# Performance work log

Measured on AMD Instinct MI355X. Metric: run time of the kernel, lower is better.

Reference implementation:

```python
import jax, jax.numpy as jnp
import numpy as np


def setup_inputs() -> dict:
    key = jax.random.key(0)
    ks = jax.random.split(key, 8)
    B, T, H, Hu = 128, 64, 1024, 512
    MJW = 64                    # max_jump_width
    J = 2 * MJW + 1             # size_jump_width_set_nn = 129
    N = 2 * T                   # HMM states (word states + null states)
    I = 64                      # source sentence length
    sc = 0.02
    return {
        "y_hidden": jax.random.normal(ks[0], (B, T, H), jnp.float32),
        # emission probs p(source word i | state s), strictly positive for log
        "emission": jax.random.uniform(ks[1], (B, N, I), jnp.float32, 1e-4, 1.0),
        "source_lengths": jax.random.randint(ks[2], (B,), 1, I + 1),
        "W1": jax.random.normal(ks[3], (H, Hu), jnp.float32) * sc,
        "b1": jnp.zeros((Hu,), jnp.float32),
        "W2": jax.random.normal(ks[4], (Hu, J), jnp.float32) * sc,
        "b2": jnp.zeros((J,), jnp.float32),
        "W3": jax.random.normal(ks[5], (Hu, 1), jnp.float32) * sc,
        "b3": jnp.zeros((1,), jnp.float32),
        "max_jump_width": MJW,
    }


def _build_transition(y_hidden, W1, b1, W2, b2, W3, b3, mjw):
    # Dense(tanh) -> Dense softmax jump-width distribution + Dense sigmoid p0
    B, T, _ = y_hidden.shape
    ts = jnp.tanh(y_hidden @ W1 + b1)                       # [B,T,Hu]
    jw = jax.nn.softmax(ts @ W2 + b2, axis=-1)              # [B,T,J]
    p0 = jax.nn.sigmoid(jnp.squeeze(ts @ W3 + b3, -1))      # [B,T]
    r = jnp.arange(T)
    # banded gather: transition[i, j] = jw[i, mjw + j - i]
    band_idx = mjw + r[None, :] - r[:, None]                # [T,T], in [0, J)
    band = jnp.take_along_axis(jw, band_idx[None], axis=2)  # [B,T,T]
    diag_p0 = jnp.eye(T, dtype=jw.dtype) * p0[:, :, None]   # [B,T,T]
    top = jnp.concatenate([band, diag_p0], axis=2)          # [B,T,2T]
    return jnp.concatenate([top, top], axis=1)              # [B,2T,2T]


def _forward_alignment(transition, emission, source_lengths):
    # Faithful translation of the tf.scan forward algorithm. tf.scan with no
    # initializer uses elems[0] as the initial accumulator and emits it as
    # output[0] (log part = ones, so the [0,0] element is 1.0).
    B, N, I = emission.shape
    em = jnp.transpose(emission, (2, 0, 1))                 # [I,B,N]
    alpha0 = jnp.broadcast_to(em[0][:, None, :], (B, N, N)) # rows all equal e_0
    L0 = jnp.ones((B,), emission.dtype)

    def step(carry, e):
        alpha, L = carry                                    # [B,N,N], [B]
        yi = e[:, None, :]                                  # rows of yi_prob identical
        m1 = jnp.matmul(alpha, transition)                  # [B,N,N]
        tmp = m1 * yi
        tmp = tmp / jnp.sum(tmp, axis=2, keepdims=True)     # row-normalized alpha
        m2 = jnp.matmul(transition, alpha) * yi             # [B,N,N]
        max_j = jnp.max(m2, axis=-1)[:, 0]                  # gather row 0 -> [B]
        state_prev = jnp.sum(m1, axis=1)                    # [B,N]
        state = jnp.log(e) + jnp.log(state_prev) - max_j[:, None]
        state_log = jnp.log(jnp.sum(jnp.exp(state), axis=-1))
        L_new = L + state_log + max_j                       # [B]
        return (tmp, L_new), L_new

    (_, _), logs = jax.lax.scan(step, (alpha0, L0), em[1:])  # [I-1,B]
    logs = jnp.concatenate([L0[None], logs], axis=0).T       # [B,I]
    idx = (source_lengths - 1)[:, None]
    return jnp.take_along_axis(logs, idx, axis=1)[:, 0]      # [B]


def reference(y_hidden, emission, source_lengths, W1, b1, W2, b2, W3, b3, max_jump_width):
    transition = _build_transition(y_hidden, W1, b1, W2, b2, W3, b3, max_jump_width)
    return _forward_alignment(transition, emission, source_lengths)
```

## Files before the change

kernel.cpp:

```cpp
#include <hip/hip_runtime.h>
#include <hip/hip_bf16.h>

typedef float f32x4 __attribute__((ext_vector_type(4)));
typedef __bf16 bf16x8 __attribute__((ext_vector_type(8)));
typedef unsigned short u16;

#define OFF_W1T  0u
#define OFF_W23B 1048576u
#define OFF_TS   1196032u

static __device__ __forceinline__ u16 f2bf(float x) {
    __bf16 h = (__bf16)x;
    return __builtin_bit_cast(u16, h);
}

__device__ __forceinline__ void gload16(const void* g, void* l) {
    __builtin_amdgcn_global_load_lds(
        (const __attribute__((address_space(1))) void*)g,
        (__attribute__((address_space(3))) void*)l,
        16, 0, 0);
}

__global__ __launch_bounds__(256) void prep_kernel(
    const float* __restrict__ W1, const float* __restrict__ W2,
    const float* __restrict__ W3,
    __bf16* __restrict__ W1T, __bf16* __restrict__ W23B)
{
    const int t = threadIdx.x;
    if (blockIdx.x < 128) {
        __shared__ __bf16 lds_t[64][72];
        const int kt = blockIdx.x >> 3, nt = blockIdx.x & 7;
        const int k0 = kt * 64, n0 = nt * 64;
        {
            const int kr = t >> 2, c0 = (t & 3) * 16;
            const float* src = W1 + (size_t)(k0 + kr) * 512 + n0 + c0;
            #pragma unroll
            for (int q = 0; q < 4; ++q) {
                float4 v = *(const float4*)(src + q * 4);
                lds_t[kr][c0 + q * 4 + 0] = (__bf16)v.x;
                lds_t[kr][c0 + q * 4 + 1] = (__bf16)v.y;
                lds_t[kr][c0 + q * 4 + 2] = (__bf16)v.z;
                lds_t[kr][c0 + q * 4 + 3] = (__bf16)v.w;
            }
        }
        __syncthreads();
        {
            const int nr = t >> 2, kc = (t & 3) * 16;
            bf16x8 o0, o1;
            #pragma unroll
            for (int j = 0; j < 8; ++j) o0[j] = lds_t[kc + j][nr];
            #pragma unroll
            for (int j = 0; j < 8; ++j) o1[j] = lds_t[kc + 8 + j][nr];
            __bf16* dst = W1T + (size_t)(n0 + nr) * 1024 + k0 + kc;
            *(bf16x8*)(dst)     = o0;
            *(bf16x8*)(dst + 8) = o1;
        }
    } else {
        int g = (blockIdx.x - 128) * 256 + t;
        if (g < 9216) {
            int n = g >> 6;
            int k8 = (g & 63) * 8;
            bf16x8 v;
            #pragma unroll
            for (int j = 0; j < 8; ++j) {
                int k = k8 + j;
                float x = 0.0f;
                if (n < 129) x = W2[(size_t)k * 129 + n];
                else if (n == 129) x = W3[k];
                v[j] = (__bf16)x;
            }
            int kk = k8 >> 5, lg = (k8 >> 3) & 3, ct = n >> 4, lr = n & 15;
            *(bf16x8*)&W23B[(((size_t)(kk * 9 + ct)) * 64 + lg * 16 + lr) * 8] = v;
        }
    }
}

__global__ __launch_bounds__(256, 2) void gemm1_kernel(
    const float* __restrict__ Y, const __bf16* __restrict__ W1T,
    const float* __restrict__ b1, u16* __restrict__ ts)
{
    __shared__ float  As[3][64 * 32];
    __shared__ __bf16 Bs[3][128 * 32];
    const int tid = threadIdx.x;
    const int m0 = blockIdx.x * 64, n0 = blockIdx.y * 128;
    const int wid = tid >> 6, lane = tid & 63;
    const int wr = wid >> 1, wc = wid & 1;
    const int lr = lane & 15, lg = lane >> 4;

    const int al = lane >> 3;
    const int au = (lane & 7) ^ al;
    const float* yA0 = Y + (size_t)(m0 + (wid * 2 + 0) * 8 + al) * 1024 + au * 4;
    const float* yA1 = Y + (size_t)(m0 + (wid * 2 + 1) * 8 + al) * 1024 + au * 4;
    const int bl = lane >> 2;
    const int bu = (lane & 3) ^ (bl & 3);
    const __bf16* wB0 = W1T + (size_t)(n0 + (wid * 2 + 0) * 16 + bl) * 1024 + bu * 8;
    const __bf16* wB1 = W1T + (size_t)(n0 + (wid * 2 + 1) * 16 + bl) * 1024 + bu * 8;

    f32x4 acc[2][4];
    #pragma unroll
    for (int m = 0; m < 2; m++)
        #pragma unroll
        for (int n = 0; n < 4; n++) { f32x4 z = {0.f,0.f,0.f,0.f}; acc[m][n] = z; }

#define STAGE(buf, kt) do { \
    gload16(yA0 + (kt) * 32, &As[buf][(wid * 2 + 0) * 256]); \
    gload16(yA1 + (kt) * 32, &As[buf][(wid * 2 + 1) * 256]); \
    gload16(wB0 + (kt) * 32, &Bs[buf][(wid * 2 + 0) * 512]); \
    gload16(wB1 + (kt) * 32, &Bs[buf][(wid * 2 + 1) * 512]); \
} while (0)

#define COMPUTE(buf) do { \
    bf16x8 af[2]; bf16x8 bfr[4]; \
    _Pragma("unroll") \
    for (int m = 0; m < 2; ++m) { \
        const int row = wr * 32 + m * 16 + lr; \
        const int r7 = row & 7; \
        float4 h0 = *(const float4*)&As[buf][row * 32 + (((lg * 2 + 0) ^ r7) * 4)]; \
        float4 h1 = *(const float4*)&As[buf][row * 32 + (((lg * 2 + 1) ^ r7) * 4)]; \
        bf16x8 tt; \
        tt[0]=(__bf16)h0.x; tt[1]=(__bf16)h0.y; tt[2]=(__bf16)h0.z; tt[3]=(__bf16)h0.w; \
        tt[4]=(__bf16)h1.x; tt[5]=(__bf16)h1.y; tt[6]=(__bf16)h1.z; tt[7]=(__bf16)h1.w; \
        af[m] = tt; \
    } \
    _Pragma("unroll") \
    for (int n = 0; n < 4; ++n) { \
        const int rowb = wc * 64 + n * 16 + lr; \
        bfr[n] = *(const bf16x8*)&Bs[buf][rowb * 32 + ((lg ^ (rowb & 3)) * 8)]; \
    } \
    __builtin_amdgcn_s_setprio(1); \
    _Pragma("unroll") \
    for (int m = 0; m < 2; ++m) \
        _Pragma("unroll") \
        for (int n = 0; n < 4; ++n) \
            acc[m][n] = __builtin_amdgcn_mfma_f32_16x16x32_bf16(af[m], bfr[n], acc[m][n], 0, 0, 0); \
    __builtin_amdgcn_s_setprio(0); \
} while (0)

#define KSTEP(buf, kt, VM, DO_STAGE) do { \
    asm volatile("s_waitcnt vmcnt(" #VM ")" ::: "memory"); \
    __builtin_amdgcn_s_barrier(); \
    COMPUTE(buf); \
    asm volatile("s_waitcnt lgkmcnt(0)" ::: "memory"); \
    __builtin_amdgcn_s_barrier(); \
    if (DO_STAGE) STAGE(buf, (kt) + 3); \
} while (0)

    STAGE(0, 0); STAGE(1, 1); STAGE(2, 2);
    #pragma unroll 1
    for (int base = 0; base < 27; base += 3) {
        KSTEP(0, base + 0, 8, 1);
        KSTEP(1, base + 1, 8, 1);
        KSTEP(2, base + 2, 8, 1);
    }
    KSTEP(0, 27, 8, 1);
    KSTEP(1, 28, 8, 1);
    KSTEP(2, 29, 8, 0);
    KSTEP(0, 30, 4, 0);
    KSTEP(1, 31, 0, 0);

    #pragma unroll
    for (int m = 0; m < 2; m++) {
        #pragma unroll
        for (int n = 0; n < 4; n++) {
            int col = n0 + wc * 64 + n * 16 + lr;
            float bias = b1[col];
            #pragma unroll
            for (int j = 0; j < 4; j++) {
                int row = m0 + wr * 32 + m * 16 + lg * 4 + j;
                float v = tanhf(acc[m][n][j] + bias);
                ts[(size_t)row * 512 + col] = f2bf(v);
            }
        }
    }
#undef STAGE
#undef COMPUTE
#undef KSTEP
}

__global__ __launch_bounds__(256, 1) void gemm2_recur_kernel(
    const u16* __restrict__ ts, const u16* __restrict__ W23B,
    const float* __restrict__ b2, const float* __restrict__ b3,
    const float* __restrict__ em, const int* __restrict__ slen,
    float* __restrict__ out)
{
    __shared__ float jwT_s[64][65];
    __shared__ float em_s[128][65];
    __shared__ float p0_s[64];
    __shared__ f32x4 a_bc4[16];
    const int b = blockIdx.x;
    const int tid = threadIdx.x;
    const int w = tid >> 6, lane = tid & 63;
    const int lr = lane & 15, lg = lane >> 4;
    const int r0 = b * 64 + w * 16;

    {
        const float4* eg = (const float4*)(em + (size_t)b * 8192);
        #pragma unroll
        for (int q = 0; q < 8; ++q) {
            int i4 = tid + q * 256;
            float4 v = eg[i4];
            int base = i4 * 4; int n = base >> 6; int ii = base & 63;
            em_s[n][ii] = v.x; em_s[n][ii + 1] = v.y; em_s[n][ii + 2] = v.z; em_s[n][ii + 3] = v.w;
        }
    }

    f32x4 acc[9];
    #pragma unroll
    for (int ct = 0; ct < 9; ct++) { f32x4 z = {0.f,0.f,0.f,0.f}; acc[ct] = z; }

    #pragma unroll 4
    for (int kk = 0; kk < 16; ++kk) {
        bf16x8 a = *(const bf16x8*)(ts + (size_t)(r0 + lr) * 512 + kk * 32 + lg * 8);
        #pragma unroll
        for (int ct = 0; ct < 9; ct++) {
            bf16x8 bv = *(const bf16x8*)(W23B + ((size_t)(kk * 9 + ct) * 64 + lane) * 8);
            acc[ct] = __builtin_amdgcn_mfma_f32_16x16x32_bf16(a, bv, acc[ct], 0, 0, 0);
        }
    }

    float b3v = b3[0];
    #pragma unroll
    for (int j = 0; j < 4; j++) {
        int rloc = w * 16 + lg * 4 + j;
        float v[9];
        float mx = -1e30f;
        #pragma unroll
        for (int ct = 0; ct < 9; ct++) {
            int col = ct * 16 + lr;
            if (col < 129) { float x = acc[ct][j] + b2[col]; v[ct] = x; mx = fmaxf(mx, x); }
            else v[ct] = -1e30f;
        }
        #pragma unroll
        for (int o = 1; o < 16; o <<= 1) mx = fmaxf(mx, __shfl_xor(mx, o));
        float sum = 0.f;
        #pragma unroll
        for (int ct = 0; ct < 9; ct++) {
            int col = ct * 16 + lr;
            if (col < 129) { float e = expf(v[ct] - mx); v[ct] = e; sum += e; }
        }
        #pragma unroll
        for (int o = 1; o < 16; o <<= 1) sum += __shfl_xor(sum, o);
        float inv = 1.0f / sum;
        #pragma unroll
        for (int ct = 0; ct < 9; ct++) {
            int col = ct * 16 + lr;
            int cc = col - 64 + rloc;
            if (col < 129 && cc >= 0 && cc < 64)
                jwT_s[cc][rloc] = v[ct] * inv;
        }
        if (lr == 1) {
            float pv = acc[8][j] + b3v;
            p0_s[rloc] = 1.0f / (1.0f + expf(-pv));
        }
    }
    __syncthreads();
    if (tid >= 64) return;

    const int c = tid;
    f32x4 B0  = *(const f32x4*)&jwT_s[c][0];
    f32x4 B1  = *(const f32x4*)&jwT_s[c][4];
    f32x4 B2  = *(const f32x4*)&jwT_s[c][8];
    f32x4 B3  = *(const f32x4*)&jwT_s[c][12];
    f32x4 B4  = *(const f32x4*)&jwT_s[c][16];
    f32x4 B5  = *(const f32x4*)&jwT_s[c][20];
    f32x4 B6  = *(const f32x4*)&jwT_s[c][24];
    f32x4 B7  = *(const f32x4*)&jwT_s[c][28];
    f32x4 B8  = *(const f32x4*)&jwT_s[c][32];
    f32x4 B9  = *(const f32x4*)&jwT_s[c][36];
    f32x4 B10 = *(const f32x4*)&jwT_s[c][40];
    f32x4 B11 = *(const f32x4*)&jwT_s[c][44];
    f32x4 B12 = *(const f32x4*)&jwT_s[c][48];
    f32x4 B13 = *(const f32x4*)&jwT_s[c][52];
    f32x4 B14 = *(const f32x4*)&jwT_s[c][56];
    f32x4 B15 = *(const f32x4*)&jwT_s[c][60];
    const float p0r = p0_s[c];
    const int idx = slen[b] - 1;

    unsigned rbase = (unsigned)(uintptr_t)(__attribute__((address_space(3))) void*)&a_bc4[0];
    unsigned waddr = rbase + (unsigned)c * 4u;

    float ut = em_s[c][0] + em_s[c + 64][0];
    float Lacc = 0.f;

    #pragma unroll 1
    for (int i = 1; i <= idx; ++i) {
        float aloc = ut;
        f32x4 A0,A1,A2,A3,A4,A5,A6,A7,A8,A9,A10,A11,A12,A13,A14,A15;
        asm volatile(
            "ds_write_b32 %17, %16\n\t"
            "s_waitcnt lgkmcnt(0)\n\t"
            "ds_read_b128 %0, %18 offset:0\n\t"
            "ds_read_b128 %1, %18 offset:16\n\t"
            "ds_read_b128 %2, %18 offset:32\n\t"
            "ds_read_b128 %3, %18 offset:48\n\t"
            "ds_read_b128 %4, %18 offset:64\n\t"
            "ds_read_b128 %5, %18 offset:80\n\t"
            "ds_read_b128 %6, %18 offset:96\n\t"
            "ds_read_b128 %7, %18 offset:112\n\t"
            "ds_read_b128 %8, %18 offset:128\n\t"
            "ds_read_b128 %9, %18 offset:144\n\t"
            "ds_read_b128 %10, %18 offset:160\n\t"
            "ds_read_b128 %11, %18 offset:176\n\t"
            "ds_read_b128 %12, %18 offset:192\n\t"
            "ds_read_b128 %13, %18 offset:208\n\t"
            "ds_read_b128 %14, %18 offset:224\n\t"
            "ds_read_b128 %15, %18 offset:240\n\t"
            "s_waitcnt lgkmcnt(0)"
            : "=&v"(A0), "=&v"(A1), "=&v"(A2),  "=&v"(A3),
              "=&v"(A4), "=&v"(A5), "=&v"(A6),  "=&v"(A7),
              "=&v"(A8), "=&v"(A9), "=&v"(A10), "=&v"(A11),
              "=&v"(A12),"=&v"(A13),"=&v"(A14), "=&v"(A15)
            : "v"(ut), "v"(waddr), "v"(rbase)
            : "memory");
        float s0 = 0.f, s1 = 0.f, s2 = 0.f, s3 = 0.f;
#define ACC4(AV, BV) do { \
        s0 = fmaf((AV)[0], (BV)[0], s0); \
        s1 = fmaf((AV)[1], (BV)[1], s1); \
        s2 = fmaf((AV)[2], (BV)[2], s2); \
        s3 = fmaf((AV)[3], (BV)[3], s3); \
} while (0)
        ACC4(A0, B0);   ACC4(A1, B1);   ACC4(A2, B2);   ACC4(A3, B3);
        ACC4(A4, B4);   ACC4(A5, B5);   ACC4(A6, B6);   ACC4(A7, B7);
        ACC4(A8, B8);   ACC4(A9, B9);   ACC4(A10, B10); ACC4(A11, B11);
        ACC4(A12, B12); ACC4(A13, B13); ACC4(A14, B14); ACC4(A15, B15);
#undef ACC4
        ut = ((s0 + s1) + (s2 + s3)) * em_s[c][i] + aloc * p0r * em_s[c + 64][i];
        if (((i & 3) == 0) || (i == idx)) {
            float r = ut;
            #pragma unroll
            for (int o = 1; o < 64; o <<= 1) r += __shfl_xor(r, o);
            Lacc += __log2f(r);
            ut *= __builtin_amdgcn_rcpf(r);
        }
    }
    if (c == 0) out[b] = 1.0f + 0.6931471805599453f * (Lacc + 7.0f * (float)idx);
}

extern "C" void kernel_launch(void* const* d_in, const int* in_sizes, int n_in,
                              void* d_out, int out_size, void* d_ws, size_t ws_size,
                              hipStream_t stream)
{
    const float* Y   = (const float*)d_in[0];
    const float* em  = (const float*)d_in[1];
    const int*   sl  = (const int*)d_in[2];
    const float* W1  = (const float*)d_in[3];
    const float* b1  = (const float*)d_in[4];
    const float* W2  = (const float*)d_in[5];
    const float* b2  = (const float*)d_in[6];
    const float* W3  = (const float*)d_in[7];
    const float* b3  = (const float*)d_in[8];
    float* out = (float*)d_out;
    char* ws = (char*)d_ws;

    __bf16* W1T  = (__bf16*)(ws + OFF_W1T);
    __bf16* W23B = (__bf16*)(ws + OFF_W23B);
    u16*    ts   = (u16*)(ws + OFF_TS);

    prep_kernel<<<164, 256, 0, stream>>>(W1, W2, W3, W1T, W23B);
    dim3 g1(128, 4);
    gemm1_kernel<<<g1, 256, 0, stream>>>(Y, W1T, b1, ts);
    gemm2_recur_kernel<<<128, 256, 0, stream>>>(ts, (const u16*)W23B, b2, b3, em, sl, out);
}
```

Baseline: 83.07 us.

## Restructure pipeline: direct-load GEMM1, split band and recurrence kernels, exponent renormalization

Pre-packs W1 into an MFMA fragment layout so gemm1 loads operands straight from global memory into registers, dropping the LDS triple-buffer pipeline and its barriers. The fused gemm2+recurrence kernel is split into a band kernel that writes jw/p0 to workspace and a 64-thread recurrence kernel. Per-step renormalization now uses an exponent-bit rescale from lane 0 instead of a periodic wave reduction, log and reciprocal. This adds a kernel launch and a global round-trip, and gemm1 loses LDS staging and latency hiding.

```diff
diff --git a/kernel.cpp b/kernel.cpp
--- a/kernel.cpp
+++ b/kernel.cpp
@@ -5,58 +5,34 @@
 typedef __bf16 bf16x8 __attribute__((ext_vector_type(8)));
 typedef unsigned short u16;
 
-#define OFF_W1T  0u
+#define OFF_W1B  0u
 #define OFF_W23B 1048576u
 #define OFF_TS   1196032u
+#define OFF_JWT  9584640u
+#define OFF_P0   11681792u
 
 static __device__ __forceinline__ u16 f2bf(float x) {
     __bf16 h = (__bf16)x;
     return __builtin_bit_cast(u16, h);
 }
 
-__device__ __forceinline__ void gload16(const void* g, void* l) {
-    __builtin_amdgcn_global_load_lds(
-        (const __attribute__((address_space(1))) void*)g,
-        (__attribute__((address_space(3))) void*)l,
-        16, 0, 0);
-}
-
 __global__ __launch_bounds__(256) void prep_kernel(
     const float* __restrict__ W1, const float* __restrict__ W2,
     const float* __restrict__ W3,
-    __bf16* __restrict__ W1T, __bf16* __restrict__ W23B)
+    __bf16* __restrict__ W1B, __bf16* __restrict__ W23B)
 {
     const int t = threadIdx.x;
-    if (blockIdx.x < 128) {
-        __shared__ __bf16 lds_t[64][72];
-        const int kt = blockIdx.x >> 3, nt = blockIdx.x & 7;
-        const int k0 = kt * 64, n0 = nt * 64;
-        {
-            const int kr = t >> 2, c0 = (t & 3) * 16;
-            const float* src = W1 + (size_t)(k0 + kr) * 512 + n0 + c0;
-            #pragma unroll
-            for (int q = 0; q < 4; ++q) {
-                float4 v = *(const float4*)(src + q * 4);
-                lds_t[kr][c0 + q * 4 + 0] = (__bf16)v.x;
-                lds_t[kr][c0 + q * 4 + 1] = (__bf16)v.y;
-                lds_t[kr][c0 + q * 4 + 2] = (__bf16)v.z;
-                lds_t[kr][c0 + q * 4 + 3] = (__bf16)v.w;
-            }
-        }
-        __syncthreads();
-        {
-            const int nr = t >> 2, kc = (t & 3) * 16;
-            bf16x8 o0, o1;
-            #pragma unroll
-            for (int j = 0; j < 8; ++j) o0[j] = lds_t[kc + j][nr];
-            #pragma unroll
-            for (int j = 0; j < 8; ++j) o1[j] = lds_t[kc + 8 + j][nr];
-            __bf16* dst = W1T + (size_t)(n0 + nr) * 1024 + k0 + kc;
-            *(bf16x8*)(dst)     = o0;
-            *(bf16x8*)(dst + 8) = o1;
-        }
+    if (blockIdx.x < 256) {
+        int g = blockIdx.x * 256 + t;
+        int n = g & 511, k8 = g >> 9;
+        bf16x8 v;
+        #pragma unroll
+        for (int j = 0; j < 8; ++j)
+            v[j] = (__bf16)W1[(size_t)(k8 * 8 + j) * 512 + n];
+        int kt = k8 >> 2, lg = k8 & 3, ct = n >> 4, lr = n & 15;
+        *(bf16x8*)&W1B[(((size_t)(kt * 32 + ct)) * 64 + lg * 16 + lr) * 8] = v;
     } else {
-        int g = (blockIdx.x - 128) * 256 + t;
+        int g = (blockIdx.x - 256) * 256 + t;
         if (g < 9216) {
             int n = g >> 6;
             int k8 = (g & 63) * 8;
@@ -75,26 +51,20 @@
     }
 }
 
-__global__ __launch_bounds__(256, 2) void gemm1_kernel(
-    const float* __restrict__ Y, const __bf16* __restrict__ W1T,
+__global__ __launch_bounds__(256) void gemm1_kernel(
+    const float* __restrict__ Y, const u16* __restrict__ W1B,
     const float* __restrict__ b1, u16* __restrict__ ts)
 {
-    __shared__ float  As[3][64 * 32];
-    __shared__ __bf16 Bs[3][128 * 32];
     const int tid = threadIdx.x;
-    const int m0 = blockIdx.x * 64, n0 = blockIdx.y * 128;
+    const int m0 = blockIdx.x * 64, nb = blockIdx.y;
     const int wid = tid >> 6, lane = tid & 63;
     const int wr = wid >> 1, wc = wid & 1;
     const int lr = lane & 15, lg = lane >> 4;
 
-    const int al = lane >> 3;
-    const int au = (lane & 7) ^ al;
-    const float* yA0 = Y + (size_t)(m0 + (wid * 2 + 0) * 8 + al) * 1024 + au * 4;
-    const float* yA1 = Y + (size_t)(m0 + (wid * 2 + 1) * 8 + al) * 1024 + au * 4;
-    const int bl = lane >> 2;
-    const int bu = (lane & 3) ^ (bl & 3);
-    const __bf16* wB0 = W1T + (size_t)(n0 + (wid * 2 + 0) * 16 + bl) * 1024 + bu * 8;
-    const __bf16* wB1 = W1T + (size_t)(n0 + (wid * 2 + 1) * 16 + bl) * 1024 + bu * 8;
+    const float* ya0 = Y + (size_t)(m0 + wr * 32 + lr) * 1024 + lg * 8;
+    const float* ya1 = ya0 + (size_t)16 * 1024;
+    const int ct0 = nb * 8 + wc * 4;
+    const u16* wb = W1B + ((size_t)ct0 * 64 + lane) * 8;
 
     f32x4 acc[2][4];
     #pragma unroll
@@ -102,67 +72,37 @@
         #pragma unroll
         for (int n = 0; n < 4; n++) { f32x4 z = {0.f,0.f,0.f,0.f}; acc[m][n] = z; }
 
-#define STAGE(buf, kt) do { \
-    gload16(yA0 + (kt) * 32, &As[buf][(wid * 2 + 0) * 256]); \
-    gload16(yA1 + (kt) * 32, &As[buf][(wid * 2 + 1) * 256]); \
-    gload16(wB0 + (kt) * 32, &Bs[buf][(wid * 2 + 0) * 512]); \
-    gload16(wB1 + (kt) * 32, &Bs[buf][(wid * 2 + 1) * 512]); \
-} while (0)
-
-#define COMPUTE(buf) do { \
-    bf16x8 af[2]; bf16x8 bfr[4]; \
-    _Pragma("unroll") \
-    for (int m = 0; m < 2; ++m) { \
-        const int row = wr * 32 + m * 16 + lr; \
-        const int r7 = row & 7; \
-        float4 h0 = *(const float4*)&As[buf][row * 32 + (((lg * 2 + 0) ^ r7) * 4)]; \
-        float4 h1 = *(const float4*)&As[buf][row * 32 + (((lg * 2 + 1) ^ r7) * 4)]; \
-        bf16x8 tt; \
-        tt[0]=(__bf16)h0.x; tt[1]=(__bf16)h0.y; tt[2]=(__bf16)h0.z; tt[3]=(__bf16)h0.w; \
-        tt[4]=(__bf16)h1.x; tt[5]=(__bf16)h1.y; tt[6]=(__bf16)h1.z; tt[7]=(__bf16)h1.w; \
-        af[m] = tt; \
-    } \
-    _Pragma("unroll") \
-    for (int n = 0; n < 4; ++n) { \
-        const int rowb = wc * 64 + n * 16 + lr; \
-        bfr[n] = *(const bf16x8*)&Bs[buf][rowb * 32 + ((lg ^ (rowb & 3)) * 8)]; \
-    } \
-    __builtin_amdgcn_s_setprio(1); \
-    _Pragma("unroll") \
-    for (int m = 0; m < 2; ++m) \
-        _Pragma("unroll") \
-        for (int n = 0; n < 4; ++n) \
-            acc[m][n] = __builtin_amdgcn_mfma_f32_16x16x32_bf16(af[m], bfr[n], acc[m][n], 0, 0, 0); \
-    __builtin_amdgcn_s_setprio(0); \
-} while (0)
-
-#define KSTEP(buf, kt, VM, DO_STAGE) do { \
-    asm volatile("s_waitcnt vmcnt(" #VM ")" ::: "memory"); \
-    __builtin_amdgcn_s_barrier(); \
-    COMPUTE(buf); \
-    asm volatile("s_waitcnt lgkmcnt(0)" ::: "memory"); \
-    __builtin_amdgcn_s_barrier(); \
-    if (DO_STAGE) STAGE(buf, (kt) + 3); \
-} while (0)
-
-    STAGE(0, 0); STAGE(1, 1); STAGE(2, 2);
-    #pragma unroll 1
-    for (int base = 0; base < 27; base += 3) {
-        KSTEP(0, base + 0, 8, 1);
-        KSTEP(1, base + 1, 8, 1);
-        KSTEP(2, base + 2, 8, 1);
-    }
-    KSTEP(0, 27, 8, 1);
-    KSTEP(1, 28, 8, 1);
-    KSTEP(2, 29, 8, 0);
-    KSTEP(0, 30, 4, 0);
-    KSTEP(1, 31, 0, 0);
+    #pragma unroll 4
+    for (int kt = 0; kt < 32; ++kt) {
+        float4 p0v = *(const float4*)(ya0 + kt * 32);
+        float4 p1v = *(const float4*)(ya0 + kt * 32 + 4);
+        float4 q0v = *(const float4*)(ya1 + kt * 32);
+        float4 q1v = *(const float4*)(ya1 + kt * 32 + 4);
+        bf16x8 a0, a1;
+        a0[0]=(__bf16)p0v.x; a0[1]=(__bf16)p0v.y; a0[2]=(__bf16)p0v.z; a0[3]=(__bf16)p0v.w;
+        a0[4]=(__bf16)p1v.x; a0[5]=(__bf16)p1v.y; a0[6]=(__bf16)p1v.z; a0[7]=(__bf16)p1v.w;
+        a1[0]=(__bf16)q0v.x; a1[1]=(__bf16)q0v.y; a1[2]=(__bf16)q0v.z; a1[3]=(__bf16)q0v.w;
+        a1[4]=(__bf16)q1v.x; a1[5]=(__bf16)q1v.y; a1[6]=(__bf16)q1v.z; a1[7]=(__bf16)q1v.w;
+        const u16* wk = wb + (size_t)kt * 16384;
+        bf16x8 bf0 = *(const bf16x8*)(wk);
+        bf16x8 bf1 = *(const bf16x8*)(wk + 512);
+        bf16x8 bf2 = *(const bf16x8*)(wk + 1024);
+        bf16x8 bf3 = *(const bf16x8*)(wk + 1536);
+        acc[0][0] = __builtin_amdgcn_mfma_f32_16x16x32_bf16(a0, bf0, acc[0][0], 0, 0, 0);
+        acc[0][1] = __builtin_amdgcn_mfma_f32_16x16x32_bf16(a0, bf1, acc[0][1], 0, 0, 0);
+        acc[0][2] = __builtin_amdgcn_mfma_f32_16x16x32_bf16(a0, bf2, acc[0][2], 0, 0, 0);
+        acc[0][3] = __builtin_amdgcn_mfma_f32_16x16x32_bf16(a0, bf3, acc[0][3], 0, 0, 0);
+        acc[1][0] = __builtin_amdgcn_mfma_f32_16x16x32_bf16(a1, bf0, acc[1][0], 0, 0, 0);
+        acc[1][1] = __builtin_amdgcn_mfma_f32_16x16x32_bf16(a1, bf1, acc[1][1], 0, 0, 0);
+        acc[1][2] = __builtin_amdgcn_mfma_f32_16x16x32_bf16(a1, bf2, acc[1][2], 0, 0, 0);
+        acc[1][3] = __builtin_amdgcn_mfma_f32_16x16x32_bf16(a1, bf3, acc[1][3], 0, 0, 0);
+    }
 
     #pragma unroll
     for (int m = 0; m < 2; m++) {
         #pragma unroll
         for (int n = 0; n < 4; n++) {
-            int col = n0 + wc * 64 + n * 16 + lr;
+            int col = nb * 128 + wc * 64 + n * 16 + lr;
             float bias = b1[col];
             #pragma unroll
             for (int j = 0; j < 4; j++) {
@@ -172,38 +112,19 @@
             }
         }
     }
-#undef STAGE
-#undef COMPUTE
-#undef KSTEP
-}
-
-__global__ __launch_bounds__(256, 1) void gemm2_recur_kernel(
+}
+
+__global__ __launch_bounds__(256) void band_kernel(
     const u16* __restrict__ ts, const u16* __restrict__ W23B,
     const float* __restrict__ b2, const float* __restrict__ b3,
-    const float* __restrict__ em, const int* __restrict__ slen,
-    float* __restrict__ out)
-{
-    __shared__ float jwT_s[64][65];
-    __shared__ float em_s[128][65];
-    __shared__ float p0_s[64];
-    __shared__ f32x4 a_bc4[16];
+    float* __restrict__ jwT, float* __restrict__ p0)
+{
     const int b = blockIdx.x;
     const int tid = threadIdx.x;
     const int w = tid >> 6, lane = tid & 63;
     const int lr = lane & 15, lg = lane >> 4;
     const int r0 = b * 64 + w * 16;
 
-    {
-        const float4* eg = (const float4*)(em + (size_t)b * 8192);
-        #pragma unroll
-        for (int q = 0; q < 8; ++q) {
-            int i4 = tid + q * 256;
-            float4 v = eg[i4];
-            int base = i4 * 4; int n = base >> 6; int ii = base & 63;
-            em_s[n][ii] = v.x; em_s[n][ii + 1] = v.y; em_s[n][ii + 2] = v.z; em_s[n][ii + 3] = v.w;
-        }
-    }
-
     f32x4 acc[9];
     #pragma unroll
     for (int ct = 0; ct < 9; ct++) { f32x4 z = {0.f,0.f,0.f,0.f}; acc[ct] = z; }
@@ -246,41 +167,61 @@
             int col = ct * 16 + lr;
             int cc = col - 64 + rloc;
             if (col < 129 && cc >= 0 && cc < 64)
-                jwT_s[cc][rloc] = v[ct] * inv;
+                jwT[((size_t)b * 64 + cc) * 64 + rloc] = v[ct] * inv;
         }
         if (lr == 1) {
             float pv = acc[8][j] + b3v;
-            p0_s[rloc] = 1.0f / (1.0f + expf(-pv));
-        }
-    }
+            p0[b * 64 + rloc] = 1.0f / (1.0f + expf(-pv));
+        }
+    }
+}
+
+__global__ __launch_bounds__(64, 1) void recur_kernel(
+    const float* __restrict__ jwT, const float* __restrict__ p0g,
+    const float* __restrict__ em, const int* __restrict__ slen,
+    float* __restrict__ out)
+{
+    __shared__ float em_s[128][65];
+    __shared__ f32x4 a_bc4[16];
+    const int b = blockIdx.x, c = threadIdx.x;
+
+    const float* bb = jwT + ((size_t)b * 64 + c) * 64;
+    f32x4 B0  = *(const f32x4*)(bb + 0);
+    f32x4 B1  = *(const f32x4*)(bb + 4);
+    f32x4 B2  = *(const f32x4*)(bb + 8);
+    f32x4 B3  = *(const f32x4*)(bb + 12);
+    f32x4 B4  = *(const f32x4*)(bb + 16);
+    f32x4 B5  = *(const f32x4*)(bb + 20);
+    f32x4 B6  = *(const f32x4*)(bb + 24);
+    f32x4 B7  = *(const f32x4*)(bb + 28);
+    f32x4 B8  = *(const f32x4*)(bb + 32);
+    f32x4 B9  = *(const f32x4*)(bb + 36);
+    f32x4 B10 = *(const f32x4*)(bb + 40);
+    f32x4 B11 = *(const f32x4*)(bb + 44);
+    f32x4 B12 = *(const f32x4*)(bb + 48);
+    f32x4 B13 = *(const f32x4*)(bb + 52);
+    f32x4 B14 = *(const f32x4*)(bb + 56);
+    f32x4 B15 = *(const f32x4*)(bb + 60);
+
+    {
+        const float4* eg = (const float4*)(em + (size_t)b * 8192);
+        #pragma unroll 8
+        for (int q = 0; q < 32; ++q) {
+            int i4 = c + q * 64;
+            float4 v = eg[i4];
+            int base = i4 * 4; int n = base >> 6; int ii = base & 63;
+            em_s[n][ii] = v.x; em_s[n][ii + 1] = v.y; em_s[n][ii + 2] = v.z; em_s[n][ii + 3] = v.w;
+        }
+    }
+    const float p0r = p0g[b * 64 + c];
+    const int idx = slen[b] - 1;
     __syncthreads();
-    if (tid >= 64) return;
-
-    const int c = tid;
-    f32x4 B0  = *(const f32x4*)&jwT_s[c][0];
-    f32x4 B1  = *(const f32x4*)&jwT_s[c][4];
-    f32x4 B2  = *(const f32x4*)&jwT_s[c][8];
-    f32x4 B3  = *(const f32x4*)&jwT_s[c][12];
-    f32x4 B4  = *(const f32x4*)&jwT_s[c][16];
-    f32x4 B5  = *(const f32x4*)&jwT_s[c][20];
-    f32x4 B6  = *(const f32x4*)&jwT_s[c][24];
-    f32x4 B7  = *(const f32x4*)&jwT_s[c][28];
-    f32x4 B8  = *(const f32x4*)&jwT_s[c][32];
-    f32x4 B9  = *(const f32x4*)&jwT_s[c][36];
-    f32x4 B10 = *(const f32x4*)&jwT_s[c][40];
-    f32x4 B11 = *(const f32x4*)&jwT_s[c][44];
-    f32x4 B12 = *(const f32x4*)&jwT_s[c][48];
-    f32x4 B13 = *(const f32x4*)&jwT_s[c][52];
-    f32x4 B14 = *(const f32x4*)&jwT_s[c][56];
-    f32x4 B15 = *(const f32x4*)&jwT_s[c][60];
-    const float p0r = p0_s[c];
-    const int idx = slen[b] - 1;
+
+    float ut = em_s[c][0] + em_s[c + 64][0];
+    int Eacc = 0;
 
     unsigned rbase = (unsigned)(uintptr_t)(__attribute__((address_space(3))) void*)&a_bc4[0];
     unsigned waddr = rbase + (unsigned)c * 4u;
-
-    float ut = em_s[c][0] + em_s[c + 64][0];
-    float Lacc = 0.f;
 
     #pragma unroll 1
     for (int i = 1; i <= idx; ++i) {
@@ -325,15 +266,20 @@
         ACC4(A12, B12); ACC4(A13, B13); ACC4(A14, B14); ACC4(A15, B15);
 #undef ACC4
         ut = ((s0 + s1) + (s2 + s3)) * em_s[c][i] + aloc * p0r * em_s[c + 64][i];
-        if (((i & 3) == 0) || (i == idx)) {
-            float r = ut;
-            #pragma unroll
-            for (int o = 1; o < 64; o <<= 1) r += __shfl_xor(r, o);
-            Lacc += __log2f(r);
-            ut *= __builtin_amdgcn_rcpf(r);
-        }
-    }
-    if (c == 0) out[b] = 1.0f + 0.6931471805599453f * (Lacc + 7.0f * (float)idx);
+        int bits = __builtin_amdgcn_readfirstlane(__float_as_int(ut));
+        int ef = (bits >> 23) & 255;
+        Eacc += ef - 127;
+        ut *= __int_as_float((254 - ef) << 23);
+    }
+    float r = ut;
+    #pragma unroll
+    for (int o = 1; o < 64; o <<= 1) r += __shfl_xor(r, o);
+    if (c == 0) {
+        float res = 1.0f;
+        if (idx > 0)
+            res = 1.0f + 0.6931471805599453f * ((float)Eacc + __log2f(r) + 7.0f * (float)idx);
+        out[b] = res;
+    }
 }
 
 extern "C" void kernel_launch(void* const* d_in, const int* in_sizes, int n_in,
@@ -352,12 +298,15 @@
     float* out = (float*)d_out;
     char* ws = (char*)d_ws;
 
-    __bf16* W1T  = (__bf16*)(ws + OFF_W1T);
+    __bf16* W1B  = (__bf16*)(ws + OFF_W1B);
     __bf16* W23B = (__bf16*)(ws + OFF_W23B);
     u16*    ts   = (u16*)(ws + OFF_TS);
-
-    prep_kernel<<<164, 256, 0, stream>>>(W1, W2, W3, W1T, W23B);
+    float*  jwT  = (float*)(ws + OFF_JWT);
+    float*  p0   = (float*)(ws + OFF_P0);
+
+    prep_kernel<<<292, 256, 0, stream>>>(W1, W2, W3, W1B, W23B);
     dim3 g1(128, 4);
-    gemm1_kernel<<<g1, 256, 0, stream>>>(Y, W1T, b1, ts);
-    gemm2_recur_kernel<<<128, 256, 0, stream>>>(ts, (const u16*)W23B, b2, b3, em, sl, out);
-}
+    gemm1_kernel<<<g1, 256, 0, stream>>>(Y, (const u16*)W1B, b1, ts);
+    band_kernel<<<128, 256, 0, stream>>>(ts, (const u16*)W23B, b2, b3, jwT, p0);
+    recur_kernel<<<128, 64, 0, stream>>>(jwT, p0, em, sl, out);
+}
```

After: 104.6 us. +25.9%, slower.
